# Kernel tuning notes

Hardware: AMD Instinct MI355X
Metric: run time of the kernel (lower is better)

## Reference

```python
import jax, jax.numpy as jnp
import numpy as np

N = 40000
E = 640000
IN_FEATS = 128
OUT_FEATS = 64
K = 8
FACTOR_DIM = OUT_FEATS // K  # 8
ITERATIONS = 3
TAU = 1.0
LEAKY_SLOPE = 0.01  # torch nn.LeakyReLU default


def setup_inputs() -> dict:
    key = jax.random.key(0)
    k1, k2, k3 = jax.random.split(key, 3)
    x = jax.random.normal(k1, (N, IN_FEATS), dtype=jnp.float32)
    # xavier_normal_ with gain=1.414: std = gain * sqrt(2 / (fan_in + fan_out))
    std = 1.414 * np.sqrt(2.0 / (IN_FEATS + OUT_FEATS))
    weight = jax.random.normal(k2, (IN_FEATS, OUT_FEATS), dtype=jnp.float32) * std
    bias = jnp.zeros((OUT_FEATS,), dtype=jnp.float32)
    edge_index = jax.random.randint(k3, (2, E), 0, N, dtype=jnp.int32)
    return {"x": x, "weight": weight, "bias": bias, "edge_index": edge_index}


def _l2norm(h):
    # h / ||h||_2 along last dim (no eps, matching torch code)
    return h / jnp.sqrt((h * h).sum(-1, keepdims=True))


def reference(x, weight, bias, edge_index):
    num_nodes = x.shape[0]
    src = edge_index[0]  # scatter target / softmax segment node
    dst = edge_index[1]  # gathered neighbor node

    h = jax.nn.leaky_relu(x @ weight + bias, LEAKY_SLOPE)          # [N, out]
    # split into K factors of FACTOR_DIM: [N, K, d]
    h = h.reshape(num_nodes, K, FACTOR_DIM)
    h_normed = _l2norm(h)                                           # [N, K, d]

    h_src = h_normed
    h_dst = h_normed
    for _ in range(ITERATIONS):
        feat_nbr = h_src[dst]                                       # [E, K, d]
        s = (h_dst[src] * feat_nbr).sum(-1) / TAU                   # [E, K]
        # segment softmax over edges grouped by src node
        smax = jax.ops.segment_max(s, src, num_segments=num_nodes)  # [N, K]
        ex = jnp.exp(s - smax[src])                                 # [E, K]
        denom = jax.ops.segment_sum(ex, src, num_segments=num_nodes)
        alpha = ex / denom[src]                                     # [E, K]
        msg = feat_nbr * alpha[..., None]                           # [E, K, d]
        node_attr = jax.ops.segment_sum(msg, src, num_segments=num_nodes)
        node_attr = node_attr + h_normed                            # [N, K, d]
        h_dst = _l2norm(node_attr)
    return h_dst.reshape(num_nodes, -1)                             # [N, out]
```

## Files before the change

kernel.cpp:

```cpp
#include <hip/hip_runtime.h>
#include <math.h>

#define NN   40000
#define EE   640000
#define INF_ 128
#define OUTF 64
#define SLOTS 64

#define NBUCK 313
#define NCOLS 157
#define NBINS (NBUCK * NCOLS)
#define SCANA_BLOCKS ((NBINS + 255) / 256)
#define NG4  (EE / 4)

typedef float f2 __attribute__((ext_vector_type(2)));

__device__ __forceinline__ f2 pkfma(f2 a, f2 b, f2 c) {
    return __builtin_elementwise_fma(a, b, c);
}
__device__ __forceinline__ f2 shf2(f2 a, int m) {
    f2 b; b.x = __shfl_xor(a.x, m); b.y = __shfl_xor(a.y, m); return b;
}
__device__ __forceinline__ f2 bfpair(unsigned u) {
    f2 c;
    c.x = __uint_as_float(u << 16);
    c.y = __uint_as_float(u & 0xffff0000u);
    return c;
}
__device__ __forceinline__ unsigned short f2bf(float f) {
    unsigned u = __float_as_uint(f);
    return (unsigned short)((u + 0x7fffu + ((u >> 16) & 1u)) >> 16);
}


__global__ __launch_bounds__(256) void count_gemm_k(
        const float* __restrict__ x, const float* __restrict__ w,
        const float* __restrict__ bias, float* __restrict__ hn,
        unsigned short* __restrict__ hn16,
        const int4* __restrict__ src4, int* __restrict__ binsT,
        uchar4* __restrict__ lrank4) {
    __shared__ float wl[INF_ * OUTF];
    __shared__ float xl[4][8 * 132];

    if (blockIdx.x < NCOLS) {
        int b = blockIdx.x;
        int* lbin = (int*)wl;
        for (int i = threadIdx.x; i < NBUCK; i += 256) lbin[i] = 0;
        __syncthreads();
#pragma unroll
        for (int rnd = 0; rnd < 4; ++rnd) {
            int gi = b * 1024 + rnd * 256 + threadIdx.x;
            if (gi < NG4) {
                int4 s = src4[gi];
                uchar4 lr;
                lr.x = (unsigned char)atomicAdd(&lbin[s.x >> 7], 1);
                lr.y = (unsigned char)atomicAdd(&lbin[s.y >> 7], 1);
                lr.z = (unsigned char)atomicAdd(&lbin[s.z >> 7], 1);
                lr.w = (unsigned char)atomicAdd(&lbin[s.w >> 7], 1);
                lrank4[gi] = lr;
            }
        }
        __syncthreads();
        for (int u = threadIdx.x; u < NBUCK; u += 256) binsT[u * NCOLS + b] = lbin[u];
        return;
    }

    for (int i = threadIdx.x; i < INF_ * OUTF; i += 256) wl[i] = w[i];

    int wv = threadIdx.x >> 6;
    int l  = threadIdx.x & 63;
    int q  = l >> 4;
    int rr = l & 15;
    float4 bv = ((const float4*)bias)[rr];
    int srow = l >> 5;
    int scol = (l & 31) * 4;

    int nb = ((blockIdx.x - NCOLS) * 4 + wv) * 16;

#pragma unroll
    for (int h = 0; h < 2; ++h) {
        int n0 = nb + h * 8;
        {
            const float4* xs = (const float4*)(x + (size_t)n0 * INF_);
#pragma unroll
            for (int j = 0; j < 4; ++j) {
                float4 v = xs[j * 64 + l];
                *(float4*)&xl[wv][(j * 2 + srow) * 132 + scol] = v;
            }
        }
        if (h == 0) __syncthreads();
        float4 a0 = bv, a1 = bv;
        const float* x0 = &xl[wv][q * 132];
        const float* x1 = &xl[wv][(q + 4) * 132];
#pragma unroll 4
        for (int i = 0; i < INF_; ++i) {
            float4 w4 = ((const float4*)wl)[i * 16 + rr];
            float xv0 = x0[i], xv1 = x1[i];
            a0.x = fmaf(xv0, w4.x, a0.x); a0.y = fmaf(xv0, w4.y, a0.y);
            a0.z = fmaf(xv0, w4.z, a0.z); a0.w = fmaf(xv0, w4.w, a0.w);
            a1.x = fmaf(xv1, w4.x, a1.x); a1.y = fmaf(xv1, w4.y, a1.y);
            a1.z = fmaf(xv1, w4.z, a1.z); a1.w = fmaf(xv1, w4.w, a1.w);
        }
        a0.x = a0.x > 0.f ? a0.x : 0.01f * a0.x;
        a0.y = a0.y > 0.f ? a0.y : 0.01f * a0.y;
        a0.z = a0.z > 0.f ? a0.z : 0.01f * a0.z;
        a0.w = a0.w > 0.f ? a0.w : 0.01f * a0.w;
        a1.x = a1.x > 0.f ? a1.x : 0.01f * a1.x;
        a1.y = a1.y > 0.f ? a1.y : 0.01f * a1.y;
        a1.z = a1.z > 0.f ? a1.z : 0.01f * a1.z;
        a1.w = a1.w > 0.f ? a1.w : 0.01f * a1.w;
        float s0 = a0.x*a0.x + a0.y*a0.y + a0.z*a0.z + a0.w*a0.w;
        float s1 = a1.x*a1.x + a1.y*a1.y + a1.z*a1.z + a1.w*a1.w;
        s0 += __shfl_xor(s0, 1);
        s1 += __shfl_xor(s1, 1);
        float v0 = rsqrtf(s0), v1 = rsqrtf(s1);
        float4 o0 = make_float4(a0.x*v0, a0.y*v0, a0.z*v0, a0.w*v0);
        float4 o1 = make_float4(a1.x*v1, a1.y*v1, a1.z*v1, a1.w*v1);
        ((float4*)hn)[(size_t)(n0 + q) * 16 + rr] = o0;
        ((float4*)hn)[(size_t)(n0 + 4 + q) * 16 + rr] = o1;
        ushort4 u0, u1;
        u0.x = f2bf(o0.x); u0.y = f2bf(o0.y); u0.z = f2bf(o0.z); u0.w = f2bf(o0.w);
        u1.x = f2bf(o1.x); u1.y = f2bf(o1.y); u1.z = f2bf(o1.z); u1.w = f2bf(o1.w);
        ((ushort4*)hn16)[(size_t)(n0 + q) * 16 + rr] = u0;
        ((ushort4*)hn16)[(size_t)(n0 + 4 + q) * 16 + rr] = u1;
    }
}


__global__ void scanA_k(const int* __restrict__ binsT, int* __restrict__ excl,
                        int* __restrict__ bsum) {
    __shared__ int tmp[256];
    int i = blockIdx.x * 256 + threadIdx.x;
    int v = (i < NBINS) ? binsT[i] : 0;
    tmp[threadIdx.x] = v;
    __syncthreads();
    for (int off = 1; off < 256; off <<= 1) {
        int t = (threadIdx.x >= off) ? tmp[threadIdx.x - off] : 0;
        __syncthreads();
        tmp[threadIdx.x] += t;
        __syncthreads();
    }
    if (i < NBINS) excl[i] = tmp[threadIdx.x] - v;
    if (threadIdx.x == 255) bsum[blockIdx.x] = tmp[255];
}

__device__ __forceinline__ void spine_scan(const int* __restrict__ bsum, int* spine) {
    int v = (threadIdx.x < SCANA_BLOCKS) ? bsum[threadIdx.x] : 0;
    spine[threadIdx.x] = v;
    __syncthreads();
    for (int off = 1; off < 256; off <<= 1) {
        int t = (threadIdx.x >= off) ? spine[threadIdx.x - off] : 0;
        __syncthreads();
        spine[threadIdx.x] += t;
        __syncthreads();
    }
    spine[threadIdx.x] -= v;
    __syncthreads();
}


__global__ __launch_bounds__(256) void part_k(const int4* __restrict__ src4,
                                              const int4* __restrict__ dst4,
                                              const uchar4* __restrict__ lrank4,
                                              const int* __restrict__ excl,
                                              const int* __restrict__ bsum,
                                              unsigned* __restrict__ part) {
    __shared__ int spine[256];
    spine_scan(bsum, spine);

    int b = blockIdx.x;
#pragma unroll
    for (int rnd = 0; rnd < 4; ++rnd) {
        int gi = b * 1024 + rnd * 256 + threadIdx.x;
        if (gi < NG4) {
            int4 s = src4[gi];
            int4 d = dst4[gi];
            uchar4 lr = lrank4[gi];
            int i0 = (s.x >> 7) * NCOLS + b;
            int i1 = (s.y >> 7) * NCOLS + b;
            int i2 = (s.z >> 7) * NCOLS + b;
            int i3 = (s.w >> 7) * NCOLS + b;
            part[excl[i0] + spine[i0 >> 8] + lr.x] = ((unsigned)d.x << 7) | (unsigned)(s.x & 127);
            part[excl[i1] + spine[i1 >> 8] + lr.y] = ((unsigned)d.y << 7) | (unsigned)(s.y & 127);
            part[excl[i2] + spine[i2 >> 8] + lr.z] = ((unsigned)d.z << 7) | (unsigned)(s.z & 127);
            part[excl[i3] + spine[i3 >> 8] + lr.w] = ((unsigned)d.w << 7) | (unsigned)(s.w & 127);
        }
    }
}


__global__ __launch_bounds__(256) void attn_build_k(const uint4* __restrict__ hg,
                                                    const float* __restrict__ hnf,
                                                    float* __restrict__ out,
                                                    const unsigned* __restrict__ part,
                                                    const int* __restrict__ excl,
                                                    const int* __restrict__ bsum) {
    __shared__ unsigned short csr_l[32][SLOTS];
    __shared__ int cnt[32];
    __shared__ int spine[256];

    spine_scan(bsum, spine);

    int u = blockIdx.x >> 2;
    int c = blockIdx.x & 3;
    if (threadIdx.x < 32) cnt[threadIdx.x] = 0;
    __syncthreads();

    int iu = u * NCOLS;
    int beg = excl[iu] + spine[iu >> 8];
    int end = EE;
    if (u + 1 < NBUCK) {
        int iv = (u + 1) * NCOLS;
        end = excl[iv] + spine[iv >> 8];
    }
    for (int e = beg + threadIdx.x; e < end; e += 256) {
        unsigned p = part[e];
        int lo = (int)(p & 127u);
        if ((lo >> 5) == c) {
            int lr = atomicAdd(&cnt[lo & 31], 1);
            if (lr < SLOTS) csr_l[lo & 31][lr] = (unsigned short)(p >> 7);
        }
    }
    __syncthreads();

    int wv = threadIdx.x >> 6;
    int l  = threadIdx.x & 63;
    int pp_ = l >> 5, q = (l >> 3) & 3, r = l & 7;
    int nbase = u * 128 + c * 32;

#pragma unroll 1
    for (int pass = 0; pass < 4; ++pass) {
        int ln = pass * 8 + wv * 2 + pp_;
        int n  = nbase + ln;
        if (n >= NN) continue;

        const unsigned short* row = csr_l[ln];
        int deg = min(cnt[ln], SLOTS);

        bool k0 = q      < deg;
        bool k1 = q + 4  < deg;
        bool k2 = q + 8  < deg;
        bool k3 = q + 12 < deg;
        bool k4 = q + 16 < deg;
        bool k5 = q + 20 < deg;
        bool k6 = q + 24 < deg;
        bool k7 = q + 28 < deg;
        unsigned i0 = min((unsigned)row[q     ], NN - 1u);
        unsigned i1 = min((unsigned)row[q +  4], NN - 1u);
        unsigned i2 = min((unsigned)row[q +  8], NN - 1u);
        unsigned i3 = min((unsigned)row[q + 12], NN - 1u);
        unsigned i4 = min((unsigned)row[q + 16], NN - 1u);
        unsigned i5 = min((unsigned)row[q + 20], NN - 1u);
        unsigned i6 = min((unsigned)row[q + 24], NN - 1u);
        unsigned i7 = min((unsigned)row[q + 28], NN - 1u);
        uint4 g0 = hg[(size_t)i0 * 8 + r];
        uint4 g1 = hg[(size_t)i1 * 8 + r];
        uint4 g2 = hg[(size_t)i2 * 8 + r];
        uint4 g3 = hg[(size_t)i3 * 8 + r];
        uint4 g4 = hg[(size_t)i4 * 8 + r];
        uint4 g5 = hg[(size_t)i5 * 8 + r];
        uint4 g6 = hg[(size_t)i6 * 8 + r];
        uint4 g7 = hg[(size_t)i7 * 8 + r];

        f2 e0c0 = bfpair(g0.x), e0c1 = bfpair(g0.y), e0c2 = bfpair(g0.z), e0c3 = bfpair(g0.w);
        f2 e1c0 = bfpair(g1.x), e1c1 = bfpair(g1.y), e1c2 = bfpair(g1.z), e1c3 = bfpair(g1.w);
        f2 e2c0 = bfpair(g2.x), e2c1 = bfpair(g2.y), e2c2 = bfpair(g2.z), e2c3 = bfpair(g2.w);
        f2 e3c0 = bfpair(g3.x), e3c1 = bfpair(g3.y), e3c2 = bfpair(g3.z), e3c3 = bfpair(g3.w);
        f2 e4c0 = bfpair(g4.x), e4c1 = bfpair(g4.y), e4c2 = bfpair(g4.z), e4c3 = bfpair(g4.w);
        f2 e5c0 = bfpair(g5.x), e5c1 = bfpair(g5.y), e5c2 = bfpair(g5.z), e5c3 = bfpair(g5.w);
        f2 e6c0 = bfpair(g6.x), e6c1 = bfpair(g6.y), e6c2 = bfpair(g6.z), e6c3 = bfpair(g6.w);
        f2 e7c0 = bfpair(g7.x), e7c1 = bfpair(g7.y), e7c2 = bfpair(g7.z), e7c3 = bfpair(g7.w);

        const float4* hs4 = (const float4*)(hnf + (size_t)n * OUTF + r * 8);
        float4 ha = hs4[0], hb = hs4[1];
        f2 hs01 = {ha.x, ha.y}, hs23 = {ha.z, ha.w};
        f2 hs45 = {hb.x, hb.y}, hs67 = {hb.z, hb.w};
        f2 hd01 = hs01, hd23 = hs23, hd45 = hs45, hd67 = hs67;

        for (int it = 0; it < 3; ++it) {
            float ssum = 0.f;
            f2 A0 = {0.f, 0.f}, A1 = A0, A2 = A0, A3 = A0;

            auto proc = [&](f2 c0, f2 c1, f2 c2, f2 c3, bool ok) {
                f2 d = c0 * hd01;
                d = pkfma(c1, hd23, d);
                d = pkfma(c2, hd45, d);
                d = pkfma(c3, hd67, d);
                float dd = d.x + d.y;
                float ex = ok ? __expf(dd) : 0.f;
                ssum += ex;
                f2 exv = {ex, ex};
                A0 = pkfma(c0, exv, A0);
                A1 = pkfma(c1, exv, A1);
                A2 = pkfma(c2, exv, A2);
                A3 = pkfma(c3, exv, A3);
            };

            proc(e0c0, e0c1, e0c2, e0c3, k0);
            proc(e1c0, e1c1, e1c2, e1c3, k1);
            proc(e2c0, e2c1, e2c2, e2c3, k2);
            proc(e3c0, e3c1, e3c2, e3c3, k3);
            proc(e4c0, e4c1, e4c2, e4c3, k4);
            proc(e5c0, e5c1, e5c2, e5c3, k5);
            proc(e6c0, e6c1, e6c2, e6c3, k6);
            proc(e7c0, e7c1, e7c2, e7c3, k7);

            for (int e = 32 + q; e < deg; e += 4) {
                unsigned ii = min((unsigned)row[e], NN - 1u);
                uint4 g = hg[(size_t)ii * 8 + r];
                proc(bfpair(g.x), bfpair(g.y), bfpair(g.z), bfpair(g.w), true);
            }

#pragma unroll
            for (int m = 8; m < 32; m <<= 1) {
                ssum += __shfl_xor(ssum, m);
                A0 += shf2(A0, m);
                A1 += shf2(A1, m);
                A2 += shf2(A2, m);
                A3 += shf2(A3, m);
            }

            float rs = (ssum > 0.f) ? 1.f / ssum : 0.f;
            f2 rsv = {rs, rs};
            f2 t01 = pkfma(A0, rsv, hs01);
            f2 t23 = pkfma(A1, rsv, hs23);
            f2 t45 = pkfma(A2, rsv, hs45);
            f2 t67 = pkfma(A3, rsv, hs67);
            f2 d = t01 * t01;
            d = pkfma(t23, t23, d);
            d = pkfma(t45, t45, d);
            d = pkfma(t67, t67, d);
            float inv = rsqrtf(d.x + d.y);
            f2 iv = {inv, inv};
            hd01 = t01 * iv; hd23 = t23 * iv; hd45 = t45 * iv; hd67 = t67 * iv;
        }

        if (q == 0) {
            float4* o4 = (float4*)(out + (size_t)n * OUTF + r * 8);
            o4[0] = make_float4(hd01.x, hd01.y, hd23.x, hd23.y);
            o4[1] = make_float4(hd45.x, hd45.y, hd67.x, hd67.y);
        }
    }
}


extern "C" void kernel_launch(void* const* d_in, const int* in_sizes, int n_in,
                              void* d_out, int out_size, void* d_ws, size_t ws_size,
                              hipStream_t stream) {
    const float* x    = (const float*)d_in[0];
    const float* w    = (const float*)d_in[1];
    const float* bias = (const float*)d_in[2];
    const int*   ei   = (const int*)d_in[3];
    const int*   src  = ei;
    const int*   dst  = ei + EE;
    float* out = (float*)d_out;

    char* ws = (char*)d_ws;
    size_t off = 0;
    float*          hn    = (float*)(ws + off);          off += (size_t)NN * OUTF * 4;
    unsigned short* hn16  = (unsigned short*)(ws + off); off += (size_t)NN * OUTF * 2;
    int*            binsT = (int*)(ws + off);            off += (size_t)NBINS * 4 + 12;
    int*            excl  = (int*)(ws + off);            off += (size_t)NBINS * 4 + 12;
    int*            bsum  = (int*)(ws + off);            off += 1024;
    uchar4*         lrank = (uchar4*)(ws + off);         off += (size_t)EE;
    unsigned*       part  = (unsigned*)(ws + off);       off += (size_t)EE * 4;
    (void)ws_size; (void)in_sizes; (void)n_in; (void)out_size;

    count_gemm_k<<<NCOLS + 625, 256, 0, stream>>>(
        x, w, bias, hn, hn16, (const int4*)src, binsT, lrank);

    scanA_k<<<SCANA_BLOCKS, 256, 0, stream>>>(binsT, excl, bsum);

    part_k<<<NCOLS, 256, 0, stream>>>((const int4*)src, (const int4*)dst,
                                      (const uchar4*)lrank, excl, bsum, part);

    attn_build_k<<<NBUCK * 4, 256, 0, stream>>>((const uint4*)hn16, hn, out,
                                                part, excl, bsum);
}
```

Measured before the change: 68.49 us.

## Replace scan-based edge partition with fixed-capacity per-bin segments

The prefix-scan kernel and the partition kernel are removed. The counting blocks now write packed edges straight into fixed-capacity slots (CAP=40) for each (bucket, column) bin, and the attention kernel reads those slots, masked by the per-bin counts. This cuts two kernel launches and their global scan passes. In exchange the attention kernel scans a padded region per bucket, which means more memory reads, and any edges past the capacity of a bin are silently dropped, so correctness depends on the edge distribution staying evenly spread.

Result: no change. 69.86 us (+2.0%).

```diff
diff --git a/kernel.cpp b/kernel.cpp
--- a/kernel.cpp
+++ b/kernel.cpp
@@ -10,7 +10,7 @@
 #define NBUCK 313
 #define NCOLS 157
 #define NBINS (NBUCK * NCOLS)
-#define SCANA_BLOCKS ((NBINS + 255) / 256)
+#define CAP  40
 #define NG4  (EE / 4)
 
 typedef float f2 __attribute__((ext_vector_type(2)));
@@ -37,8 +37,8 @@
         const float* __restrict__ x, const float* __restrict__ w,
         const float* __restrict__ bias, float* __restrict__ hn,
         unsigned short* __restrict__ hn16,
-        const int4* __restrict__ src4, int* __restrict__ binsT,
-        uchar4* __restrict__ lrank4) {
+        const int4* __restrict__ src4, const int4* __restrict__ dst4,
+        int* __restrict__ binsT, unsigned* __restrict__ csr_seg) {
     __shared__ float wl[INF_ * OUTF];
     __shared__ float xl[4][8 * 132];
 
@@ -52,12 +52,16 @@
             int gi = b * 1024 + rnd * 256 + threadIdx.x;
             if (gi < NG4) {
                 int4 s = src4[gi];
-                uchar4 lr;
-                lr.x = (unsigned char)atomicAdd(&lbin[s.x >> 7], 1);
-                lr.y = (unsigned char)atomicAdd(&lbin[s.y >> 7], 1);
-                lr.z = (unsigned char)atomicAdd(&lbin[s.z >> 7], 1);
-                lr.w = (unsigned char)atomicAdd(&lbin[s.w >> 7], 1);
-                lrank4[gi] = lr;
+                int4 d = dst4[gi];
+                int u0 = s.x >> 7, u1 = s.y >> 7, u2 = s.z >> 7, u3 = s.w >> 7;
+                int r0 = atomicAdd(&lbin[u0], 1);
+                int r1 = atomicAdd(&lbin[u1], 1);
+                int r2 = atomicAdd(&lbin[u2], 1);
+                int r3 = atomicAdd(&lbin[u3], 1);
+                if (r0 < CAP) csr_seg[(u0 * NCOLS + b) * CAP + r0] = ((unsigned)d.x << 7) | (unsigned)(s.x & 127);
+                if (r1 < CAP) csr_seg[(u1 * NCOLS + b) * CAP + r1] = ((unsigned)d.y << 7) | (unsigned)(s.y & 127);
+                if (r2 < CAP) csr_seg[(u2 * NCOLS + b) * CAP + r2] = ((unsigned)d.z << 7) | (unsigned)(s.z & 127);
+                if (r3 < CAP) csr_seg[(u3 * NCOLS + b) * CAP + r3] = ((unsigned)d.w << 7) | (unsigned)(s.w & 127);
             }
         }
         __syncthreads();
@@ -127,98 +131,33 @@
 }
 
 
-__global__ void scanA_k(const int* __restrict__ binsT, int* __restrict__ excl,
-                        int* __restrict__ bsum) {
-    __shared__ int tmp[256];
-    int i = blockIdx.x * 256 + threadIdx.x;
-    int v = (i < NBINS) ? binsT[i] : 0;
-    tmp[threadIdx.x] = v;
-    __syncthreads();
-    for (int off = 1; off < 256; off <<= 1) {
-        int t = (threadIdx.x >= off) ? tmp[threadIdx.x - off] : 0;
-        __syncthreads();
-        tmp[threadIdx.x] += t;
-        __syncthreads();
-    }
-    if (i < NBINS) excl[i] = tmp[threadIdx.x] - v;
-    if (threadIdx.x == 255) bsum[blockIdx.x] = tmp[255];
-}
-
-__device__ __forceinline__ void spine_scan(const int* __restrict__ bsum, int* spine) {
-    int v = (threadIdx.x < SCANA_BLOCKS) ? bsum[threadIdx.x] : 0;
-    spine[threadIdx.x] = v;
-    __syncthreads();
-    for (int off = 1; off < 256; off <<= 1) {
-        int t = (threadIdx.x >= off) ? spine[threadIdx.x - off] : 0;
-        __syncthreads();
-        spine[threadIdx.x] += t;
-        __syncthreads();
-    }
-    spine[threadIdx.x] -= v;
-    __syncthreads();
-}
-
-
-__global__ __launch_bounds__(256) void part_k(const int4* __restrict__ src4,
-                                              const int4* __restrict__ dst4,
-                                              const uchar4* __restrict__ lrank4,
-                                              const int* __restrict__ excl,
-                                              const int* __restrict__ bsum,
-                                              unsigned* __restrict__ part) {
-    __shared__ int spine[256];
-    spine_scan(bsum, spine);
-
-    int b = blockIdx.x;
-#pragma unroll
-    for (int rnd = 0; rnd < 4; ++rnd) {
-        int gi = b * 1024 + rnd * 256 + threadIdx.x;
-        if (gi < NG4) {
-            int4 s = src4[gi];
-            int4 d = dst4[gi];
-            uchar4 lr = lrank4[gi];
-            int i0 = (s.x >> 7) * NCOLS + b;
-            int i1 = (s.y >> 7) * NCOLS + b;
-            int i2 = (s.z >> 7) * NCOLS + b;
-            int i3 = (s.w >> 7) * NCOLS + b;
-            part[excl[i0] + spine[i0 >> 8] + lr.x] = ((unsigned)d.x << 7) | (unsigned)(s.x & 127);
-            part[excl[i1] + spine[i1 >> 8] + lr.y] = ((unsigned)d.y << 7) | (unsigned)(s.y & 127);
-            part[excl[i2] + spine[i2 >> 8] + lr.z] = ((unsigned)d.z << 7) | (unsigned)(s.z & 127);
-            part[excl[i3] + spine[i3 >> 8] + lr.w] = ((unsigned)d.w << 7) | (unsigned)(s.w & 127);
-        }
-    }
-}
-
-
 __global__ __launch_bounds__(256) void attn_build_k(const uint4* __restrict__ hg,
                                                     const float* __restrict__ hnf,
                                                     float* __restrict__ out,
-                                                    const unsigned* __restrict__ part,
-                                                    const int* __restrict__ excl,
-                                                    const int* __restrict__ bsum) {
+                                                    const unsigned* __restrict__ csr_seg,
+                                                    const int* __restrict__ binsT) {
     __shared__ unsigned short csr_l[32][SLOTS];
     __shared__ int cnt[32];
-    __shared__ int spine[256];
-
-    spine_scan(bsum, spine);
+    __shared__ int cntc[NCOLS];
 
     int u = blockIdx.x >> 2;
     int c = blockIdx.x & 3;
     if (threadIdx.x < 32) cnt[threadIdx.x] = 0;
+    for (int b = threadIdx.x; b < NCOLS; b += 256)
+        cntc[b] = min(binsT[u * NCOLS + b], CAP);
     __syncthreads();
 
-    int iu = u * NCOLS;
-    int beg = excl[iu] + spine[iu >> 8];
-    int end = EE;
-    if (u + 1 < NBUCK) {
-        int iv = (u + 1) * NCOLS;
-        end = excl[iv] + spine[iv >> 8];
-    }
-    for (int e = beg + threadIdx.x; e < end; e += 256) {
-        unsigned p = part[e];
-        int lo = (int)(p & 127u);
-        if ((lo >> 5) == c) {
-            int lr = atomicAdd(&cnt[lo & 31], 1);
-            if (lr < SLOTS) csr_l[lo & 31][lr] = (unsigned short)(p >> 7);
+    const unsigned* seg = csr_seg + (size_t)u * NCOLS * CAP;
+    for (int idx = threadIdx.x; idx < NCOLS * CAP; idx += 256) {
+        int b = idx / CAP;
+        int s = idx - b * CAP;
+        unsigned p = seg[idx];
+        if (s < cntc[b]) {
+            int lo = (int)(p & 127u);
+            if ((lo >> 5) == c) {
+                int lr = atomicAdd(&cnt[lo & 31], 1);
+                if (lr < SLOTS) csr_l[lo & 31][lr] = (unsigned short)(p >> 7);
+            }
         }
     }
     __syncthreads();
@@ -357,23 +296,15 @@
 
     char* ws = (char*)d_ws;
     size_t off = 0;
-    float*          hn    = (float*)(ws + off);          off += (size_t)NN * OUTF * 4;
-    unsigned short* hn16  = (unsigned short*)(ws + off); off += (size_t)NN * OUTF * 2;
-    int*            binsT = (int*)(ws + off);            off += (size_t)NBINS * 4 + 12;
-    int*            excl  = (int*)(ws + off);            off += (size_t)NBINS * 4 + 12;
-    int*            bsum  = (int*)(ws + off);            off += 1024;
-    uchar4*         lrank = (uchar4*)(ws + off);         off += (size_t)EE;
-    unsigned*       part  = (unsigned*)(ws + off);       off += (size_t)EE * 4;
+    float*          hn      = (float*)(ws + off);          off += (size_t)NN * OUTF * 4;
+    unsigned short* hn16    = (unsigned short*)(ws + off); off += (size_t)NN * OUTF * 2;
+    int*            binsT   = (int*)(ws + off);            off += (size_t)NBINS * 4 + 12;
+    unsigned*       csr_seg = (unsigned*)(ws + off);       off += (size_t)NBINS * CAP * 4;
     (void)ws_size; (void)in_sizes; (void)n_in; (void)out_size;
 
     count_gemm_k<<<NCOLS + 625, 256, 0, stream>>>(
-        x, w, bias, hn, hn16, (const int4*)src, binsT, lrank);
-
-    scanA_k<<<SCANA_BLOCKS, 256, 0, stream>>>(binsT, excl, bsum);
-
-    part_k<<<NCOLS, 256, 0, stream>>>((const int4*)src, (const int4*)dst,
-                                      (const uchar4*)lrank, excl, bsum, part);
+        x, w, bias, hn, hn16, (const int4*)src, (const int4*)dst, binsT, csr_seg);
 
     attn_build_k<<<NBUCK * 4, 256, 0, stream>>>((const uint4*)hn16, hn, out,
-                                                part, excl, bsum);
-}
+                                                csr_seg, binsT);
+}
```

## Bucket edges by 32-node groups so each attention block reads only its edges

Applied to the files above, without the earlier changes.

The counting-sort partition now bins edges by source>>5 (1250 buckets of 32 nodes) over 40 column blocks, instead of source>>7 (313 buckets) over 157 columns. As a result, each attn_build block owns exactly one bucket and no longer scans a 128-node bucket four times while discarding three quarters of the edges. The scatter kernel is flattened to one int4 of edges per thread across 625 blocks, which raises parallelism. The cost is that counting uses only 40 blocks, each looping 16 rounds with more LDS bins.

Result: faster. 66.15 us (-3.4%).

```diff
diff --git a/kernel.cpp b/kernel.cpp
--- a/kernel.cpp
+++ b/kernel.cpp
@@ -7,9 +7,9 @@
 #define OUTF 64
 #define SLOTS 64
 
-#define NBUCK 313
-#define NCOLS 157
-#define NBINS (NBUCK * NCOLS)
+#define NB32  1250
+#define NCOLS 40
+#define NBINS (NB32 * NCOLS)
 #define SCANA_BLOCKS ((NBINS + 255) / 256)
 #define NG4  (EE / 4)
 
@@ -45,23 +45,23 @@
     if (blockIdx.x < NCOLS) {
         int b = blockIdx.x;
         int* lbin = (int*)wl;
-        for (int i = threadIdx.x; i < NBUCK; i += 256) lbin[i] = 0;
+        for (int i = threadIdx.x; i < NB32; i += 256) lbin[i] = 0;
         __syncthreads();
 #pragma unroll
-        for (int rnd = 0; rnd < 4; ++rnd) {
-            int gi = b * 1024 + rnd * 256 + threadIdx.x;
+        for (int rnd = 0; rnd < 16; ++rnd) {
+            int gi = b * 4096 + rnd * 256 + threadIdx.x;
             if (gi < NG4) {
                 int4 s = src4[gi];
                 uchar4 lr;
-                lr.x = (unsigned char)atomicAdd(&lbin[s.x >> 7], 1);
-                lr.y = (unsigned char)atomicAdd(&lbin[s.y >> 7], 1);
-                lr.z = (unsigned char)atomicAdd(&lbin[s.z >> 7], 1);
-                lr.w = (unsigned char)atomicAdd(&lbin[s.w >> 7], 1);
+                lr.x = (unsigned char)atomicAdd(&lbin[s.x >> 5], 1);
+                lr.y = (unsigned char)atomicAdd(&lbin[s.y >> 5], 1);
+                lr.z = (unsigned char)atomicAdd(&lbin[s.z >> 5], 1);
+                lr.w = (unsigned char)atomicAdd(&lbin[s.w >> 5], 1);
                 lrank4[gi] = lr;
             }
         }
         __syncthreads();
-        for (int u = threadIdx.x; u < NBUCK; u += 256) binsT[u * NCOLS + b] = lbin[u];
+        for (int u = threadIdx.x; u < NB32; u += 256) binsT[u * NCOLS + b] = lbin[u];
         return;
     }
 
@@ -168,24 +168,19 @@
     __shared__ int spine[256];
     spine_scan(bsum, spine);
 
-    int b = blockIdx.x;
-#pragma unroll
-    for (int rnd = 0; rnd < 4; ++rnd) {
-        int gi = b * 1024 + rnd * 256 + threadIdx.x;
-        if (gi < NG4) {
-            int4 s = src4[gi];
-            int4 d = dst4[gi];
-            uchar4 lr = lrank4[gi];
-            int i0 = (s.x >> 7) * NCOLS + b;
-            int i1 = (s.y >> 7) * NCOLS + b;
-            int i2 = (s.z >> 7) * NCOLS + b;
-            int i3 = (s.w >> 7) * NCOLS + b;
-            part[excl[i0] + spine[i0 >> 8] + lr.x] = ((unsigned)d.x << 7) | (unsigned)(s.x & 127);
-            part[excl[i1] + spine[i1 >> 8] + lr.y] = ((unsigned)d.y << 7) | (unsigned)(s.y & 127);
-            part[excl[i2] + spine[i2 >> 8] + lr.z] = ((unsigned)d.z << 7) | (unsigned)(s.z & 127);
-            part[excl[i3] + spine[i3 >> 8] + lr.w] = ((unsigned)d.w << 7) | (unsigned)(s.w & 127);
-        }
-    }
+    int gi = blockIdx.x * 256 + threadIdx.x;
+    int b  = gi >> 12;
+    int4 s = src4[gi];
+    int4 d = dst4[gi];
+    uchar4 lr = lrank4[gi];
+    int i0 = (s.x >> 5) * NCOLS + b;
+    int i1 = (s.y >> 5) * NCOLS + b;
+    int i2 = (s.z >> 5) * NCOLS + b;
+    int i3 = (s.w >> 5) * NCOLS + b;
+    part[excl[i0] + spine[i0 >> 8] + lr.x] = ((unsigned)d.x << 5) | (unsigned)(s.x & 31);
+    part[excl[i1] + spine[i1 >> 8] + lr.y] = ((unsigned)d.y << 5) | (unsigned)(s.y & 31);
+    part[excl[i2] + spine[i2 >> 8] + lr.z] = ((unsigned)d.z << 5) | (unsigned)(s.z & 31);
+    part[excl[i3] + spine[i3 >> 8] + lr.w] = ((unsigned)d.w << 5) | (unsigned)(s.w & 31);
 }
 
 
@@ -201,32 +196,29 @@
 
     spine_scan(bsum, spine);
 
-    int u = blockIdx.x >> 2;
-    int c = blockIdx.x & 3;
+    int nb = blockIdx.x;
     if (threadIdx.x < 32) cnt[threadIdx.x] = 0;
     __syncthreads();
 
-    int iu = u * NCOLS;
+    int iu = nb * NCOLS;
     int beg = excl[iu] + spine[iu >> 8];
     int end = EE;
-    if (u + 1 < NBUCK) {
-        int iv = (u + 1) * NCOLS;
+    if (nb + 1 < NB32) {
+        int iv = (nb + 1) * NCOLS;
         end = excl[iv] + spine[iv >> 8];
     }
     for (int e = beg + threadIdx.x; e < end; e += 256) {
         unsigned p = part[e];
-        int lo = (int)(p & 127u);
-        if ((lo >> 5) == c) {
-            int lr = atomicAdd(&cnt[lo & 31], 1);
-            if (lr < SLOTS) csr_l[lo & 31][lr] = (unsigned short)(p >> 7);
-        }
+        int lo = (int)(p & 31u);
+        int lr = atomicAdd(&cnt[lo], 1);
+        if (lr < SLOTS) csr_l[lo][lr] = (unsigned short)(p >> 5);
     }
     __syncthreads();
 
     int wv = threadIdx.x >> 6;
     int l  = threadIdx.x & 63;
     int pp_ = l >> 5, q = (l >> 3) & 3, r = l & 7;
-    int nbase = u * 128 + c * 32;
+    int nbase = nb * 32;
 
 #pragma unroll 1
     for (int pass = 0; pass < 4; ++pass) {
@@ -359,8 +351,8 @@
     size_t off = 0;
     float*          hn    = (float*)(ws + off);          off += (size_t)NN * OUTF * 4;
     unsigned short* hn16  = (unsigned short*)(ws + off); off += (size_t)NN * OUTF * 2;
-    int*            binsT = (int*)(ws + off);            off += (size_t)NBINS * 4 + 12;
-    int*            excl  = (int*)(ws + off);            off += (size_t)NBINS * 4 + 12;
+    int*            binsT = (int*)(ws + off);            off += (size_t)NBINS * 4 + 16;
+    int*            excl  = (int*)(ws + off);            off += (size_t)NBINS * 4 + 16;
     int*            bsum  = (int*)(ws + off);            off += 1024;
     uchar4*         lrank = (uchar4*)(ws + off);         off += (size_t)EE;
     unsigned*       part  = (unsigned*)(ws + off);       off += (size_t)EE * 4;
@@ -371,9 +363,9 @@
 
     scanA_k<<<SCANA_BLOCKS, 256, 0, stream>>>(binsT, excl, bsum);
 
-    part_k<<<NCOLS, 256, 0, stream>>>((const int4*)src, (const int4*)dst,
-                                      (const uchar4*)lrank, excl, bsum, part);
-
-    attn_build_k<<<NBUCK * 4, 256, 0, stream>>>((const uint4*)hn16, hn, out,
-                                                part, excl, bsum);
-}
+    part_k<<<NG4 / 256, 256, 0, stream>>>((const int4*)src, (const int4*)dst,
+                                          (const uchar4*)lrank, excl, bsum, part);
+
+    attn_build_k<<<NB32, 256, 0, stream>>>((const uint4*)hn16, hn, out,
+                                           part, excl, bsum);
+}
```
